# Kernel tuning notes

Measured on AMD Instinct MI355X. Metric: run time of the kernel, lower is better.

Reference implementation:

```python
import jax, jax.numpy as jnp
import numpy as np

DIMS = [128, 256, 512, 512]
RES = [64, 32, 16, 8]
B = 2
HEADS = 8
DH = 64
INNER = HEADS * DH  # 512


def setup_inputs() -> dict:
    key = jax.random.key(0)
    d = {}
    ctr = [0]
    def nk():
        ctr[0] += 1
        return jax.random.fold_in(key, ctr[0])
    for i, (c, r) in enumerate(zip(DIMS, RES)):
        for nm in ("ml_c", "ml_r", "fl_r"):
            d[f"{nm}{i}"] = jax.random.normal(nk(), (B, c, r, r), dtype=jnp.float32)
        for p in ("q", "k", "v"):
            d[f"w{p}{i}"] = jax.random.normal(nk(), (c, INNER), dtype=jnp.float32) * (c ** -0.5)
            d[f"b{p}{i}"] = jnp.zeros((INNER,), jnp.float32)
        d[f"wo{i}"] = jax.random.normal(nk(), (INNER, c), dtype=jnp.float32) * (INNER ** -0.5)
        d[f"bo{i}"] = jnp.zeros((c,), jnp.float32)
    return d


def _layer(xc, xr, xf, wq, bq, wk, bk, wv, bv, wo, bo):
    # xc/xr/xf: (B, C, H, W)
    Bb, C, H, W = xf.shape
    L = H * W
    flat = lambda t: t.reshape(Bb, C, L).transpose(0, 2, 1)          # (B, L, C)
    split = lambda t: t.reshape(Bb, L, HEADS, DH).transpose(0, 2, 1, 3)  # (B, h, L, d)
    q = split(flat(xc) @ wq + bq)
    k = split(flat(xr) @ wk + bk)
    v = split(flat(xf) @ wv + bv)
    attn = jax.nn.softmax(jnp.einsum('bhid,bhjd->bhij', q, k) * (DH ** -0.5), axis=-1)
    out = jnp.einsum('bhij,bhjd->bhid', attn, v)                      # (B, h, L, d)
    out = out.transpose(0, 2, 1, 3).reshape(Bb, L, INNER) @ wo + bo   # (B, L, C)
    return out.reshape(Bb, H, W, C).transpose(0, 3, 1, 2)             # (B, C, H, W)


def reference(ml_c0, ml_c1, ml_c2, ml_c3, ml_r0, ml_r1, ml_r2, ml_r3,
              fl_r0, fl_r1, fl_r2, fl_r3,
              wq0, bq0, wk0, bk0, wv0, bv0, wo0, bo0,
              wq1, bq1, wk1, bk1, wv1, bv1, wo1, bo1,
              wq2, bq2, wk2, bk2, wv2, bv2, wo2, bo2,
              wq3, bq3, wk3, bk3, wv3, bv3, wo3, bo3):
    mc = (ml_c0, ml_c1, ml_c2, ml_c3)
    mr = (ml_r0, ml_r1, ml_r2, ml_r3)
    fr = (fl_r0, fl_r1, fl_r2, fl_r3)
    ps = ((wq0, bq0, wk0, bk0, wv0, bv0, wo0, bo0),
          (wq1, bq1, wk1, bk1, wv1, bv1, wo1, bo1),
          (wq2, bq2, wk2, bk2, wv2, bv2, wo2, bo2),
          (wq3, bq3, wk3, bk3, wv3, bv3, wo3, bo3))
    return tuple(_layer(mc[i], mr[i], fr[i], *ps[i]) for i in range(4))
```

## Files before the change

kernel.cpp:

```cpp
#include <hip/hip_runtime.h>


typedef __attribute__((ext_vector_type(8))) short bf16x8;
typedef __attribute__((ext_vector_type(16))) float f32x16;
typedef __attribute__((ext_vector_type(4))) unsigned u32x4;
union BW { u32x4 u; bf16x8 b; };

#if __has_builtin(__builtin_amdgcn_exp2f)
#define EXP2F(x) __builtin_amdgcn_exp2f(x)
#else
#define EXP2F(x) exp2f(x)
#endif

__device__ __forceinline__ unsigned short f2bf(float f) {
    unsigned u = __float_as_uint(f);
    u += 0x7fffu + ((u >> 16) & 1u);
    return (unsigned short)(u >> 16);
}
__device__ __forceinline__ unsigned pack_bf16(float a, float b) {
    unsigned ua = __float_as_uint(a) + 0x8000u;
    unsigned ub = __float_as_uint(b) + 0x8000u;
#if __has_builtin(__builtin_amdgcn_perm)
    return __builtin_amdgcn_perm(ub, ua, 0x07060302u);
#else
    return (ua >> 16) | (ub & 0xffff0000u);
#endif
}

struct LayerP {
    unsigned short *xct, *xrt, *xft;
    unsigned short *wqt, *wkt, *wvt;
    unsigned short *wot;
    const float *bq, *bk, *bv, *bo;
    unsigned short *Qb, *Kb, *Vb, *Obt;
    float *out;
    int L, C;
};
struct Params {
    LayerP l[4];
    int xo128[5];
    int xoA[5];
};

struct Job { const float* src; unsigned short* dst; int R, C; };
struct PrepParams { Job jobs[40]; int off[41]; int njobs; };

__device__ __forceinline__ int layer_of(int bx, const int* xo) {
    return (bx >= xo[1]) + (bx >= xo[2]) + (bx >= xo[3]);
}

__global__ __launch_bounds__(256) void prep(PrepParams P)
{
    __shared__ float T[32][33];
    int bx = blockIdx.x, j = 0;
    while (j + 1 < P.njobs && bx >= P.off[j + 1]) ++j;
    const Job job = P.jobs[j];
    const int t = bx - P.off[j];
    const int rt = job.R >> 5;
    const int tr = t % rt, tc = t / rt;

    const int tid = threadIdx.x;
    const int c = tid & 31, rb = tid >> 5;
    const float* sp = job.src + (size_t)(tr * 32 + rb) * job.C + tc * 32 + c;
#pragma unroll
    for (int i = 0; i < 4; ++i)
        T[rb + 8 * i][c] = sp[(size_t)8 * i * job.C];
    __syncthreads();

    const int cp = tid & 15, dl = tid >> 4;
#pragma unroll
    for (int ph = 0; ph < 2; ++ph) {
        int d = dl + 16 * ph;
        unsigned v = pack_bf16(T[2 * cp][d], T[2 * cp + 1][d]);
        *(unsigned*)&job.dst[(size_t)(tc * 32 + d) * job.R + tr * 32 + 2 * cp] = v;
    }
}

__device__ __forceinline__ void gemm_bt_core(
        const unsigned short* __restrict__ At, int m0, int M,
        const unsigned short* __restrict__ Wt,
        int K, unsigned short* As, unsigned short* Ws, f32x16 (&acc)[2][2])
{
    const int tid = threadIdx.x;
    const int r = tid >> 1, half = tid & 1;
    const int rm = (m0 + r < M) ? (m0 + r) : (M - 1);
    const unsigned short* ap = At + (size_t)rm * K + half * 16;
    const unsigned short* wp = Wt + (size_t)r * K + half * 16;
    const int s = (r >> 3) & 3;
    const int wb0 = r * 40 + (((half * 2)     ^ s) << 3);
    const int wb1 = r * 40 + (((half * 2 + 1) ^ s) << 3);

    const int lane = tid & 63, wave = tid >> 6;
    const int q = lane & 31, h = lane >> 5;
    const int wm = (wave & 1) * 64, wn = (wave >> 1) * 64;

#pragma unroll
    for (int i = 0; i < 2; ++i)
#pragma unroll
        for (int jn = 0; jn < 2; ++jn)
#pragma unroll
            for (int e = 0; e < 16; ++e) acc[i][jn][e] = 0.f;

    uint4 a0 = *(const uint4*)ap,       a1 = *(const uint4*)(ap + 8);
    uint4 w0 = *(const uint4*)wp,       w1 = *(const uint4*)(wp + 8);

    for (int k0 = 0; k0 < K; k0 += 32) {
        __syncthreads();
        *(uint4*)&As[wb0] = a0;  *(uint4*)&As[wb1] = a1;
        *(uint4*)&Ws[wb0] = w0;  *(uint4*)&Ws[wb1] = w1;
        __syncthreads();
        if (k0 + 32 < K) {
            a0 = *(const uint4*)(ap + k0 + 32);  a1 = *(const uint4*)(ap + k0 + 40);
            w0 = *(const uint4*)(wp + k0 + 32);  w1 = *(const uint4*)(wp + k0 + 40);
        }
#pragma unroll
        for (int c = 0; c < 2; ++c) {
            bf16x8 af[2], bf[2];
#pragma unroll
            for (int im = 0; im < 2; ++im) {
                int rr = wm + im * 32 + q;
                af[im] = *(const bf16x8*)&As[rr * 40 + ((((c << 1) | h) ^ ((rr >> 3) & 3)) << 3)];
                int rn = wn + im * 32 + q;
                bf[im] = *(const bf16x8*)&Ws[rn * 40 + ((((c << 1) | h) ^ ((rn >> 3) & 3)) << 3)];
            }
#pragma unroll
            for (int im = 0; im < 2; ++im)
#pragma unroll
                for (int in = 0; in < 2; ++in)
                    acc[im][in] = __builtin_amdgcn_mfma_f32_32x32x16_bf16(
                        af[im], bf[in], acc[im][in], 0, 0, 0);
        }
    }
}

__global__ __launch_bounds__(256) void proj_qkv(Params P)
{
    __shared__ unsigned short As[128 * 40], Ws[128 * 40];
    const int bx = blockIdx.x;
    const int layer = layer_of(bx, P.xo128);
    const LayerP lp = P.l[layer];
    const int M = lp.L, K = lp.C;
    const int m0 = (bx - P.xo128[layer]) * 128;
    const int p = blockIdx.z >> 1, b = blockIdx.z & 1;
    const int n0 = blockIdx.y * 128;

    const unsigned short* At = (p == 0 ? lp.xct : p == 1 ? lp.xrt : lp.xft)
                               + (size_t)b * M * K;
    const unsigned short* Wt = (p == 0 ? lp.wqt : p == 1 ? lp.wkt : lp.wvt)
                               + (size_t)n0 * K;
    const float* bias = (p == 0 ? lp.bq : p == 1 ? lp.bk : lp.bv);

    f32x16 acc[2][2];
    gemm_bt_core(At, m0, M, Wt, K, As, Ws, acc);

    const int tid = threadIdx.x, lane = tid & 63, wave = tid >> 6;
    const int q = lane & 31, h = lane >> 5;
    const int wm = (wave & 1) * 64, wn = (wave >> 1) * 64;
    const int bh = b * 8 + (n0 >> 6) + (wn >> 6);

#pragma unroll
    for (int im = 0; im < 2; ++im) {
        const int m_base = m0 + wm + im * 32;
        if (m_base >= M) continue;
#pragma unroll
        for (int in = 0; in < 2; ++in) {
            const int d = in * 32 + q;
            const float bvv = bias[n0 + wn + d];
            const f32x16 A = acc[im][in];
            if (p <= 1) {
                const float sc = (p == 0) ? 0.18033688f : 1.f;
                const int ck = d >> 4, hk = (d >> 3) & 1, jk = d & 7;
                unsigned short* O = (p == 0 ? lp.Qb : lp.Kb)
                                  + (size_t)bh * (M / 32) * 2048
                                  + (size_t)((m_base >> 5) * 4 + ck) * 512 + hk * 8 + jk;
#pragma unroll
                for (int rg = 0; rg < 4; ++rg)
#pragma unroll
                    for (int i = 0; i < 4; ++i)
                        O[(rg * 8 + 4 * h + i) * 16] = f2bf((A[rg * 4 + i] + bvv) * sc);
            } else {
                unsigned short* O = lp.Vb + (size_t)bh * (M / 16) * 1024;
#pragma unroll
                for (int rg = 0; rg < 4; ++rg) {
                    int kc16 = (m_base >> 4) + (rg >> 1);
                    int j16 = (rg & 1) * 8 + 4 * h;
                    uint2 vv;
                    vv.x = pack_bf16(A[rg * 4 + 0] + bvv, A[rg * 4 + 1] + bvv);
                    vv.y = pack_bf16(A[rg * 4 + 2] + bvv, A[rg * 4 + 3] + bvv);
                    *(uint2*)(O + ((size_t)kc16 * 64 + d) * 16 + j16) = vv;
                }
            }
        }
    }
}

__global__ __launch_bounds__(256, 2) void attn(Params P)
{
    __shared__ float Os[2][32][68];
    __shared__ float Ls[4][2][64];
    __shared__ float Li[32];

    const int bx = blockIdx.x;
    const int layer = layer_of(bx, P.xoA);
    const LayerP lp = P.l[layer];
    const int L = lp.L;
    const int q0 = (bx - P.xoA[layer]) * 64;
    const int bh = blockIdx.y;

    const int tid = threadIdx.x, wave = tid >> 6, lane = tid & 63;
    const int q = lane & 31, h = lane >> 5;
    const bool hb = (h != 0);

    const unsigned short* Qbase = lp.Qb + (size_t)bh * (L / 32) * 2048 + q * 16 + h * 8;
    const unsigned short* Kbase = lp.Kb + (size_t)bh * (L / 32) * 2048 + q * 16 + h * 8;
    const unsigned short* Vbase = lp.Vb + (size_t)bh * (L / 16) * 1024 + q * 16 + h * 8;

    bf16x8 qf[2][4];
#pragma unroll
    for (int g = 0; g < 2; ++g)
#pragma unroll
        for (int c = 0; c < 4; ++c)
            qf[g][c] = *(const bf16x8*)(Qbase + (size_t)(q0 / 32 + g) * 2048 + c * 512);

    f32x16 o0[2], o1[2];
#pragma unroll
    for (int g = 0; g < 2; ++g)
#pragma unroll
        for (int i = 0; i < 16; ++i) { o0[g][i] = 0.f; o1[g][i] = 0.f; }
    float lacc[2] = {0.f, 0.f};

    const int nkt = L >> 6;
    for (int kt = wave; kt < nkt; kt += 4) {
        const unsigned short* kp0 = Kbase + (size_t)(kt * 2) * 2048;
        bf16x8 ka[4], kb_[4];
#pragma unroll
        for (int c = 0; c < 4; ++c) {
            ka[c]  = *(const bf16x8*)(kp0 + c * 512);
            kb_[c] = *(const bf16x8*)(kp0 + 2048 + c * 512);
        }
        const unsigned short* vp0 = Vbase + (size_t)(kt * 4) * 1024;
        bf16x8 va[4], vb[4];
#pragma unroll
        for (int kc = 0; kc < 4; ++kc) {
            va[kc] = *(const bf16x8*)(vp0 + kc * 1024);
            vb[kc] = *(const bf16x8*)(vp0 + kc * 1024 + 512);
        }

#pragma unroll
        for (int g = 0; g < 2; ++g) {
            f32x16 st0, st1;
#pragma unroll
            for (int i = 0; i < 16; ++i) { st0[i] = 0.f; st1[i] = 0.f; }
#pragma unroll
            for (int c = 0; c < 4; ++c) {
                st0 = __builtin_amdgcn_mfma_f32_32x32x16_bf16(ka[c],  qf[g][c], st0, 0, 0, 0);
                st1 = __builtin_amdgcn_mfma_f32_32x32x16_bf16(kb_[c], qf[g][c], st1, 0, 0, 0);
            }

            float ls = 0.f;
#pragma unroll
            for (int i = 0; i < 16; ++i) {
                st0[i] = EXP2F(st0[i]); ls += st0[i];
                st1[i] = EXP2F(st1[i]); ls += st1[i];
            }
            ls += __shfl_xor(ls, 32);
            lacc[g] += ls;

            unsigned pw0[8], pw1[8];
#pragma unroll
            for (int mt = 0; mt < 2; ++mt) {
                const f32x16 sM = mt ? st1 : st0;
#pragma unroll
                for (int rg = 0; rg < 4; ++rg) {
                    pw0[mt * 4 + rg] = pack_bf16(sM[rg * 4 + 0], sM[rg * 4 + 1]);
                    pw1[mt * 4 + rg] = pack_bf16(sM[rg * 4 + 2], sM[rg * 4 + 3]);
                }
            }

#pragma unroll
            for (int kc = 0; kc < 4; ++kc) {
                const int mt = kc >> 1, rb = (kc & 1) * 2;
                unsigned ownA = hb ? pw0[mt * 4 + rb + 1] : pw0[mt * 4 + rb];
                unsigned ownB = hb ? pw1[mt * 4 + rb + 1] : pw1[mt * 4 + rb];
                unsigned srcA = hb ? pw0[mt * 4 + rb]     : pw0[mt * 4 + rb + 1];
                unsigned srcB = hb ? pw1[mt * 4 + rb]     : pw1[mt * 4 + rb + 1];
                unsigned gotA = __shfl_xor(srcA, 32);
                unsigned gotB = __shfl_xor(srcB, 32);
                BW bw;
                bw.u[0] = hb ? gotA : ownA;
                bw.u[1] = hb ? gotB : ownB;
                bw.u[2] = hb ? ownA : gotA;
                bw.u[3] = hb ? ownB : gotB;
                o0[g] = __builtin_amdgcn_mfma_f32_32x32x16_bf16(va[kc], bw.b, o0[g], 0, 0, 0);
                o1[g] = __builtin_amdgcn_mfma_f32_32x32x16_bf16(vb[kc], bw.b, o1[g], 0, 0, 0);
            }
        }
    }

    Ls[wave][0][lane] = lacc[0];
    Ls[wave][1][lane] = lacc[1];

#pragma unroll 1
    for (int g = 0; g < 2; ++g) {
        __syncthreads();
        if (wave >= 2) {
#pragma unroll
            for (int r = 0; r < 16; ++r) {
                Os[wave - 2][r][lane]      = o0[g][r];
                Os[wave - 2][16 + r][lane] = o1[g][r];
            }
        }
        __syncthreads();
        if (wave < 2) {
#pragma unroll
            for (int r = 0; r < 16; ++r) {
                Os[wave][r][lane]      += o0[g][r];
                Os[wave][16 + r][lane] += o1[g][r];
            }
        }
        __syncthreads();
        if (tid < 32)
            Li[tid] = 1.f / (Ls[0][g][tid] + Ls[1][g][tid] + Ls[2][g][tid] + Ls[3][g][tid]);
        __syncthreads();

        const int d = tid >> 2, qg = (tid & 3) * 8;
        const int dm = d & 31;
        const int hh2 = (dm >> 2) & 1;
        const int R = ((dm & 3) | ((dm >> 3) << 2)) + ((d >= 32) ? 16 : 0);
        float v[8];
#pragma unroll
        for (int j = 0; j < 8; ++j)
            v[j] = (Os[0][R][hh2 * 32 + qg + j] + Os[1][R][hh2 * 32 + qg + j]) * Li[qg + j];
        __syncthreads();
#pragma unroll
        for (int j = 0; j < 8; ++j)
            ((float*)Os)[(qg + j) * 68 + d] = v[j];
        __syncthreads();
        {
            const int qq = tid >> 3, db = (tid & 7) * 8;
            const float* xp = &((float*)Os)[qq * 68 + db];
            u32x4 pk;
            pk[0] = pack_bf16(xp[0], xp[1]);
            pk[1] = pack_bf16(xp[2], xp[3]);
            pk[2] = pack_bf16(xp[4], xp[5]);
            pk[3] = pack_bf16(xp[6], xp[7]);
            const int bb = bh >> 3, hh = bh & 7;
            const int row = q0 + g * 32 + qq;
            *(u32x4*)(lp.Obt + ((size_t)bb * L + row) * 512 + hh * 64 + db) = pk;
        }
    }
}

__global__ __launch_bounds__(256) void proj_o(Params P)
{
    const int bx = blockIdx.x;
    const int layer = layer_of(bx, P.xo128);
    const LayerP lp = P.l[layer];
    const int M = lp.L, N = lp.C;
    const int n0 = blockIdx.y * 128;
    if (n0 >= N) return;
    __shared__ unsigned short As[128 * 40], Ws[128 * 40];
    const int m0 = (bx - P.xo128[layer]) * 128;
    const int b = blockIdx.z;

    f32x16 acc[2][2];
    gemm_bt_core(lp.Obt + (size_t)b * M * 512, m0, M,
                 lp.wot + (size_t)n0 * 512, 512, As, Ws, acc);

    const int tid = threadIdx.x, lane = tid & 63, wave = tid >> 6;
    const int q = lane & 31, h = lane >> 5;
    const int wm = (wave & 1) * 64, wn = (wave >> 1) * 64;

#pragma unroll
    for (int im = 0; im < 2; ++im) {
        const int m_base = m0 + wm + im * 32;
        if (m_base >= M) continue;
#pragma unroll
        for (int in = 0; in < 2; ++in) {
            const int n = n0 + wn + in * 32 + q;
            if (n >= N) continue;
            const float bvv = lp.bo[n];
            float* O = lp.out + ((size_t)b * N + n) * M;
            const f32x16 A = acc[im][in];
#pragma unroll
            for (int rg = 0; rg < 4; ++rg) {
                float vv[4];
#pragma unroll
                for (int i = 0; i < 4; ++i) vv[i] = A[rg * 4 + i] + bvv;
                *(float4*)(O + m_base + rg * 8 + 4 * h) = *(float4*)vv;
            }
        }
    }
}

static void build_prep(PrepParams& PP, const Params& P, int first, int last)
{
    int nj = 0, off = 0;
    for (int i = first; i < last; ++i) {
        const LayerP& lp = P.l[i];
        const int C = lp.C, L = lp.L;
        unsigned short* xd[3] = { lp.xct, lp.xrt, lp.xft };
        for (int tn = 0; tn < 3; ++tn)
            for (int b = 0; b < 2; ++b) {
                Job& J = PP.jobs[nj];
                J.dst = xd[tn] + (size_t)b * L * C;
                J.src = nullptr;
                J.R = C; J.C = L;
                PP.off[nj] = off; off += (C / 32) * (L / 32); ++nj;
            }
        unsigned short* wd[3] = { lp.wqt, lp.wkt, lp.wvt };
        for (int wn = 0; wn < 3; ++wn) {
            Job& J = PP.jobs[nj];
            J.dst = wd[wn]; J.src = nullptr; J.R = C; J.C = 512;
            PP.off[nj] = off; off += (C / 32) * 16; ++nj;
        }
        Job& J = PP.jobs[nj];
        J.dst = lp.wot; J.src = nullptr; J.R = 512; J.C = C;
        PP.off[nj] = off; off += 16 * (C / 32); ++nj;
    }
    PP.njobs = nj;
    PP.off[nj] = off;
}

extern "C" void kernel_launch(void* const* d_in, const int* in_sizes, int n_in,
                              void* d_out, int out_size, void* d_ws, size_t ws_size,
                              hipStream_t stream)
{
    static const int DIMS[4] = {128, 256, 512, 512};
    static const int RES[4]  = {64, 32, 16, 8};

    char* ws = (char*)d_ws;
    float* outf = (float*)d_out;

    Params P;
    const float* srcs[4][10];
    size_t out_off = 0;

    size_t qkv_tot = 0, xt_tot = 0, obt_tot = 0, w_tot = 0;
    int Ls_[4], Cs_[4];
    for (int i = 0; i < 4; ++i) {
        Ls_[i] = RES[i] * RES[i]; Cs_[i] = DIMS[i];
        qkv_tot += (size_t)6144 * Ls_[i];
        xt_tot  += (size_t)12 * Ls_[i] * Cs_[i];
        obt_tot += (size_t)2048 * Ls_[i];
        w_tot   += (size_t)4096 * Cs_[i];
    }
    size_t r2 = (xt_tot > obt_tot) ? xt_tot : obt_tot;
    const bool fits = qkv_tot + r2 + w_tot <= ws_size;

    auto fill_layer = [&](int i, size_t qkv_base, size_t xt_base, size_t obt_base,
                          size_t w_base) {
        const int C = Cs_[i], L = Ls_[i];
        LayerP& lp = P.l[i];
        for (int t = 0; t < 10; ++t) srcs[i][t] = nullptr;
        srcs[i][0] = (const float*)d_in[i * 11 + 0];
        srcs[i][1] = (const float*)d_in[i * 11 + 1];
        srcs[i][2] = (const float*)d_in[i * 11 + 2];
        srcs[i][3] = (const float*)d_in[i * 11 + 3];
        srcs[i][4] = (const float*)d_in[i * 11 + 5];
        srcs[i][5] = (const float*)d_in[i * 11 + 7];
        srcs[i][6] = (const float*)d_in[i * 11 + 9];
        lp.bq = (const float*)d_in[i * 11 + 4];
        lp.bk = (const float*)d_in[i * 11 + 6];
        lp.bv = (const float*)d_in[i * 11 + 8];
        lp.bo = (const float*)d_in[i * 11 + 10];
        lp.Qb  = (unsigned short*)(ws + qkv_base);
        lp.Kb  = (unsigned short*)(ws + qkv_base + (size_t)2048 * L);
        lp.Vb  = (unsigned short*)(ws + qkv_base + (size_t)4096 * L);
        lp.xct = (unsigned short*)(ws + xt_base);
        lp.xrt = (unsigned short*)(ws + xt_base + (size_t)4 * L * C);
        lp.xft = (unsigned short*)(ws + xt_base + (size_t)8 * L * C);
        lp.Obt = (unsigned short*)(ws + obt_base);
        lp.wqt = (unsigned short*)(ws + w_base);
        lp.wkt = (unsigned short*)(ws + w_base + (size_t)1024 * C);
        lp.wvt = (unsigned short*)(ws + w_base + (size_t)2048 * C);
        lp.wot = (unsigned short*)(ws + w_base + (size_t)3072 * C);
        lp.out = outf + out_off;
        lp.L = L; lp.C = C;
    };

    dim3 blk(256);

    if (fits) {
        size_t qb = 0, xb = qkv_tot, ob = qkv_tot, wb = qkv_tot + r2;
        P.xo128[0] = P.xoA[0] = 0;
        for (int i = 0; i < 4; ++i) {
            fill_layer(i, qb, xb, ob, wb);
            qb += (size_t)6144 * Ls_[i];
            xb += (size_t)12 * Ls_[i] * Cs_[i];
            ob += (size_t)2048 * Ls_[i];
            wb += (size_t)4096 * Cs_[i];
            out_off += (size_t)2 * Cs_[i] * Ls_[i];
            P.xo128[i + 1] = P.xo128[i] + (Ls_[i] + 127) / 128;
            P.xoA[i + 1]   = P.xoA[i] + Ls_[i] / 64;
        }
        PrepParams PP;
        build_prep(PP, P, 0, 4);
        {
            int nj = 0;
            for (int i = 0; i < 4; ++i) {
                for (int tn = 0; tn < 3; ++tn)
                    for (int b = 0; b < 2; ++b)
                        PP.jobs[nj++].src = srcs[i][tn] + (size_t)b * Cs_[i] * Ls_[i];
                for (int wn = 0; wn < 3; ++wn) PP.jobs[nj++].src = srcs[i][3 + wn];
                PP.jobs[nj++].src = srcs[i][6];
            }
        }
        prep    <<<dim3(PP.off[PP.njobs]), blk, 0, stream>>>(PP);
        proj_qkv<<<dim3(P.xo128[4], 4, 6), blk, 0, stream>>>(P);
        attn    <<<dim3(P.xoA[4], 16, 1), blk, 0, stream>>>(P);
        proj_o  <<<dim3(P.xo128[4], 4, 2), blk, 0, stream>>>(P);
    } else {
        for (int i = 0; i < 4; ++i) {
            const int L = Ls_[i], C = Cs_[i];
            size_t qb = 0;
            size_t xb = (size_t)6144 * L;
            size_t ob = xb;
            size_t r2i = (size_t)12 * L * C;
            if ((size_t)2048 * L > r2i) r2i = (size_t)2048 * L;
            size_t wb = xb + r2i;
            fill_layer(i, qb, xb, ob, wb);
            out_off += (size_t)2 * C * L;

            Params Pi;
            Pi.l[0] = P.l[i]; Pi.l[1] = P.l[i]; Pi.l[2] = P.l[i]; Pi.l[3] = P.l[i];
            Pi.xo128[0] = 0; Pi.xoA[0] = 0;
            for (int k = 1; k < 5; ++k) {
                Pi.xo128[k] = (L + 127) / 128;
                Pi.xoA[k]   = L / 64;
            }
            PrepParams PP;
            build_prep(PP, Pi, 0, 1);
            {
                int nj = 0;
                for (int tn = 0; tn < 3; ++tn)
                    for (int b = 0; b < 2; ++b)
                        PP.jobs[nj++].src = srcs[i][tn] + (size_t)b * C * L;
                for (int wn = 0; wn < 3; ++wn) PP.jobs[nj++].src = srcs[i][3 + wn];
                PP.jobs[nj++].src = srcs[i][6];
            }
            prep    <<<dim3(PP.off[PP.njobs]), blk, 0, stream>>>(PP);
            proj_qkv<<<dim3(Pi.xo128[4], 4, 6), blk, 0, stream>>>(Pi);
            attn    <<<dim3(Pi.xoA[4], 16, 1), blk, 0, stream>>>(Pi);
            proj_o  <<<dim3(Pi.xo128[4], 4, 2), blk, 0, stream>>>(Pi);
        }
    }
}
```

Baseline: 357.3 us.

## Shrink attention query tile to 32 rows per block and regroup workspace per layer

The attention kernel now handles 32 query rows per block instead of 64. This doubles the grid, drops the per-block loop over two query groups, and raises the occupancy hint from 2 to 3 blocks. The aim is more parallelism across CUs for the small layers and lower register pressure. In exchange, every K/V tile is loaded twice as often across blocks. The host code is also restructured to pack as many layers as fit into the workspace per launch group, overlaying Obt on the transposed-input region. Kernels are templated so each launch grouping gets its own instantiation.

```diff
diff --git a/kernel.cpp b/kernel.cpp
--- a/kernel.cpp
+++ b/kernel.cpp
@@ -39,7 +39,7 @@
 struct Params {
     LayerP l[4];
     int xo128[5];
-    int xoA[5];
+    int xo32[5];
 };
 
 struct Job { const float* src; unsigned short* dst; int R, C; };
@@ -49,6 +49,7 @@
     return (bx >= xo[1]) + (bx >= xo[2]) + (bx >= xo[3]);
 }
 
+template<int TAG>
 __global__ __launch_bounds__(256) void prep(PrepParams P)
 {
     __shared__ float T[32][33];
@@ -133,6 +134,7 @@
     }
 }
 
+template<int TAG>
 __global__ __launch_bounds__(256) void proj_qkv(Params P)
 {
     __shared__ unsigned short As[128 * 40], Ws[128 * 40];
@@ -194,17 +196,18 @@
     }
 }
 
-__global__ __launch_bounds__(256, 2) void attn(Params P)
+template<int TAG>
+__global__ __launch_bounds__(256, 3) void attn(Params P)
 {
     __shared__ float Os[2][32][68];
-    __shared__ float Ls[4][2][64];
+    __shared__ float Ls[4][64];
     __shared__ float Li[32];
 
     const int bx = blockIdx.x;
-    const int layer = layer_of(bx, P.xoA);
+    const int layer = layer_of(bx, P.xo32);
     const LayerP lp = P.l[layer];
     const int L = lp.L;
-    const int q0 = (bx - P.xoA[layer]) * 64;
+    const int q0 = (bx - P.xo32[layer]) * 32;
     const int bh = blockIdx.y;
 
     const int tid = threadIdx.x, wave = tid >> 6, lane = tid & 63;
@@ -215,19 +218,15 @@
     const unsigned short* Kbase = lp.Kb + (size_t)bh * (L / 32) * 2048 + q * 16 + h * 8;
     const unsigned short* Vbase = lp.Vb + (size_t)bh * (L / 16) * 1024 + q * 16 + h * 8;
 
-    bf16x8 qf[2][4];
-#pragma unroll
-    for (int g = 0; g < 2; ++g)
-#pragma unroll
-        for (int c = 0; c < 4; ++c)
-            qf[g][c] = *(const bf16x8*)(Qbase + (size_t)(q0 / 32 + g) * 2048 + c * 512);
-
-    f32x16 o0[2], o1[2];
-#pragma unroll
-    for (int g = 0; g < 2; ++g)
-#pragma unroll
-        for (int i = 0; i < 16; ++i) { o0[g][i] = 0.f; o1[g][i] = 0.f; }
-    float lacc[2] = {0.f, 0.f};
+    bf16x8 qf[4];
+#pragma unroll
+    for (int c = 0; c < 4; ++c)
+        qf[c] = *(const bf16x8*)(Qbase + (size_t)(q0 >> 5) * 2048 + c * 512);
+
+    f32x16 o0, o1;
+#pragma unroll
+    for (int i = 0; i < 16; ++i) { o0[i] = 0.f; o1[i] = 0.f; }
+    float lacc = 0.f;
 
     const int nkt = L >> 6;
     for (int kt = wave; kt < nkt; kt += 4) {
@@ -238,6 +237,15 @@
             ka[c]  = *(const bf16x8*)(kp0 + c * 512);
             kb_[c] = *(const bf16x8*)(kp0 + 2048 + c * 512);
         }
+        f32x16 st0, st1;
+#pragma unroll
+        for (int i = 0; i < 16; ++i) { st0[i] = 0.f; st1[i] = 0.f; }
+#pragma unroll
+        for (int c = 0; c < 4; ++c) {
+            st0 = __builtin_amdgcn_mfma_f32_32x32x16_bf16(ka[c],  qf[c], st0, 0, 0, 0);
+            st1 = __builtin_amdgcn_mfma_f32_32x32x16_bf16(kb_[c], qf[c], st1, 0, 0, 0);
+        }
+
         const unsigned short* vp0 = Vbase + (size_t)(kt * 4) * 1024;
         bf16x8 va[4], vb[4];
 #pragma unroll
@@ -246,111 +254,96 @@
             vb[kc] = *(const bf16x8*)(vp0 + kc * 1024 + 512);
         }
 
-#pragma unroll
-        for (int g = 0; g < 2; ++g) {
-            f32x16 st0, st1;
-#pragma unroll
-            for (int i = 0; i < 16; ++i) { st0[i] = 0.f; st1[i] = 0.f; }
-#pragma unroll
-            for (int c = 0; c < 4; ++c) {
-                st0 = __builtin_amdgcn_mfma_f32_32x32x16_bf16(ka[c],  qf[g][c], st0, 0, 0, 0);
-                st1 = __builtin_amdgcn_mfma_f32_32x32x16_bf16(kb_[c], qf[g][c], st1, 0, 0, 0);
+        float ls = 0.f;
+#pragma unroll
+        for (int i = 0; i < 16; ++i) {
+            st0[i] = EXP2F(st0[i]); ls += st0[i];
+            st1[i] = EXP2F(st1[i]); ls += st1[i];
+        }
+        lacc += ls;
+
+        unsigned pw0[8], pw1[8];
+#pragma unroll
+        for (int mt = 0; mt < 2; ++mt) {
+            const f32x16 sM = mt ? st1 : st0;
+#pragma unroll
+            for (int rg = 0; rg < 4; ++rg) {
+                pw0[mt * 4 + rg] = pack_bf16(sM[rg * 4 + 0], sM[rg * 4 + 1]);
+                pw1[mt * 4 + rg] = pack_bf16(sM[rg * 4 + 2], sM[rg * 4 + 3]);
             }
-
-            float ls = 0.f;
-#pragma unroll
-            for (int i = 0; i < 16; ++i) {
-                st0[i] = EXP2F(st0[i]); ls += st0[i];
-                st1[i] = EXP2F(st1[i]); ls += st1[i];
-            }
-            ls += __shfl_xor(ls, 32);
-            lacc[g] += ls;
-
-            unsigned pw0[8], pw1[8];
-#pragma unroll
-            for (int mt = 0; mt < 2; ++mt) {
-                const f32x16 sM = mt ? st1 : st0;
-#pragma unroll
-                for (int rg = 0; rg < 4; ++rg) {
-                    pw0[mt * 4 + rg] = pack_bf16(sM[rg * 4 + 0], sM[rg * 4 + 1]);
-                    pw1[mt * 4 + rg] = pack_bf16(sM[rg * 4 + 2], sM[rg * 4 + 3]);
-                }
-            }
-
-#pragma unroll
-            for (int kc = 0; kc < 4; ++kc) {
-                const int mt = kc >> 1, rb = (kc & 1) * 2;
-                unsigned ownA = hb ? pw0[mt * 4 + rb + 1] : pw0[mt * 4 + rb];
-                unsigned ownB = hb ? pw1[mt * 4 + rb + 1] : pw1[mt * 4 + rb];
-                unsigned srcA = hb ? pw0[mt * 4 + rb]     : pw0[mt * 4 + rb + 1];
-                unsigned srcB = hb ? pw1[mt * 4 + rb]     : pw1[mt * 4 + rb + 1];
-                unsigned gotA = __shfl_xor(srcA, 32);
-                unsigned gotB = __shfl_xor(srcB, 32);
-                BW bw;
-                bw.u[0] = hb ? gotA : ownA;
-                bw.u[1] = hb ? gotB : ownB;
-                bw.u[2] = hb ? ownA : gotA;
-                bw.u[3] = hb ? ownB : gotB;
-                o0[g] = __builtin_amdgcn_mfma_f32_32x32x16_bf16(va[kc], bw.b, o0[g], 0, 0, 0);
-                o1[g] = __builtin_amdgcn_mfma_f32_32x32x16_bf16(vb[kc], bw.b, o1[g], 0, 0, 0);
-            }
-        }
-    }
-
-    Ls[wave][0][lane] = lacc[0];
-    Ls[wave][1][lane] = lacc[1];
-
-#pragma unroll 1
-    for (int g = 0; g < 2; ++g) {
-        __syncthreads();
-        if (wave >= 2) {
-#pragma unroll
-            for (int r = 0; r < 16; ++r) {
-                Os[wave - 2][r][lane]      = o0[g][r];
-                Os[wave - 2][16 + r][lane] = o1[g][r];
-            }
-        }
-        __syncthreads();
-        if (wave < 2) {
-#pragma unroll
-            for (int r = 0; r < 16; ++r) {
-                Os[wave][r][lane]      += o0[g][r];
-                Os[wave][16 + r][lane] += o1[g][r];
-            }
-        }
-        __syncthreads();
-        if (tid < 32)
-            Li[tid] = 1.f / (Ls[0][g][tid] + Ls[1][g][tid] + Ls[2][g][tid] + Ls[3][g][tid]);
-        __syncthreads();
-
-        const int d = tid >> 2, qg = (tid & 3) * 8;
-        const int dm = d & 31;
-        const int hh2 = (dm >> 2) & 1;
-        const int R = ((dm & 3) | ((dm >> 3) << 2)) + ((d >= 32) ? 16 : 0);
-        float v[8];
-#pragma unroll
-        for (int j = 0; j < 8; ++j)
-            v[j] = (Os[0][R][hh2 * 32 + qg + j] + Os[1][R][hh2 * 32 + qg + j]) * Li[qg + j];
-        __syncthreads();
-#pragma unroll
-        for (int j = 0; j < 8; ++j)
-            ((float*)Os)[(qg + j) * 68 + d] = v[j];
-        __syncthreads();
-        {
-            const int qq = tid >> 3, db = (tid & 7) * 8;
-            const float* xp = &((float*)Os)[qq * 68 + db];
-            u32x4 pk;
-            pk[0] = pack_bf16(xp[0], xp[1]);
-            pk[1] = pack_bf16(xp[2], xp[3]);
-            pk[2] = pack_bf16(xp[4], xp[5]);
-            pk[3] = pack_bf16(xp[6], xp[7]);
-            const int bb = bh >> 3, hh = bh & 7;
-            const int row = q0 + g * 32 + qq;
-            *(u32x4*)(lp.Obt + ((size_t)bb * L + row) * 512 + hh * 64 + db) = pk;
-        }
-    }
-}
-
+        }
+
+#pragma unroll
+        for (int kc = 0; kc < 4; ++kc) {
+            const int mt = kc >> 1, rb = (kc & 1) * 2;
+            unsigned ownA = hb ? pw0[mt * 4 + rb + 1] : pw0[mt * 4 + rb];
+            unsigned ownB = hb ? pw1[mt * 4 + rb + 1] : pw1[mt * 4 + rb];
+            unsigned srcA = hb ? pw0[mt * 4 + rb]     : pw0[mt * 4 + rb + 1];
+            unsigned srcB = hb ? pw1[mt * 4 + rb]     : pw1[mt * 4 + rb + 1];
+            unsigned gotA = __shfl_xor(srcA, 32);
+            unsigned gotB = __shfl_xor(srcB, 32);
+            BW bw;
+            bw.u[0] = hb ? gotA : ownA;
+            bw.u[1] = hb ? gotB : ownB;
+            bw.u[2] = hb ? ownA : gotA;
+            bw.u[3] = hb ? ownB : gotB;
+            o0 = __builtin_amdgcn_mfma_f32_32x32x16_bf16(va[kc], bw.b, o0, 0, 0, 0);
+            o1 = __builtin_amdgcn_mfma_f32_32x32x16_bf16(vb[kc], bw.b, o1, 0, 0, 0);
+        }
+    }
+
+    Ls[wave][lane] = lacc;
+    if (wave >= 2) {
+#pragma unroll
+        for (int r = 0; r < 16; ++r) {
+            Os[wave - 2][r][lane]      = o0[r];
+            Os[wave - 2][16 + r][lane] = o1[r];
+        }
+    }
+    __syncthreads();
+    if (wave < 2) {
+#pragma unroll
+        for (int r = 0; r < 16; ++r) {
+            Os[wave][r][lane]      += o0[r];
+            Os[wave][16 + r][lane] += o1[r];
+        }
+    }
+    __syncthreads();
+    if (tid < 32) {
+        float s = 0.f;
+#pragma unroll
+        for (int w = 0; w < 4; ++w) s += Ls[w][tid] + Ls[w][32 + tid];
+        Li[tid] = 1.f / s;
+    }
+    __syncthreads();
+
+    const int d = tid >> 2, qg = (tid & 3) * 8;
+    const int dm = d & 31;
+    const int hh2 = (dm >> 2) & 1;
+    const int R = ((dm & 3) | ((dm >> 3) << 2)) + ((d >= 32) ? 16 : 0);
+    float v[8];
+#pragma unroll
+    for (int j = 0; j < 8; ++j)
+        v[j] = (Os[0][R][hh2 * 32 + qg + j] + Os[1][R][hh2 * 32 + qg + j]) * Li[qg + j];
+    __syncthreads();
+#pragma unroll
+    for (int j = 0; j < 8; ++j)
+        ((float*)Os)[(qg + j) * 68 + d] = v[j];
+    __syncthreads();
+    {
+        const int qq = tid >> 3, db = (tid & 7) * 8;
+        const float* xp = &((float*)Os)[qq * 68 + db];
+        u32x4 pk;
+        pk[0] = pack_bf16(xp[0], xp[1]);
+        pk[1] = pack_bf16(xp[2], xp[3]);
+        pk[2] = pack_bf16(xp[4], xp[5]);
+        pk[3] = pack_bf16(xp[6], xp[7]);
+        const int bb = bh >> 3, hh = bh & 7;
+        *(u32x4*)(lp.Obt + ((size_t)bb * L + q0 + qq) * 512 + hh * 64 + db) = pk;
+    }
+}
+
+template<int TAG>
 __global__ __launch_bounds__(256) void proj_o(Params P)
 {
     const int bx = blockIdx.x;
@@ -393,35 +386,6 @@
     }
 }
 
-static void build_prep(PrepParams& PP, const Params& P, int first, int last)
-{
-    int nj = 0, off = 0;
-    for (int i = first; i < last; ++i) {
-        const LayerP& lp = P.l[i];
-        const int C = lp.C, L = lp.L;
-        unsigned short* xd[3] = { lp.xct, lp.xrt, lp.xft };
-        for (int tn = 0; tn < 3; ++tn)
-            for (int b = 0; b < 2; ++b) {
-                Job& J = PP.jobs[nj];
-                J.dst = xd[tn] + (size_t)b * L * C;
-                J.src = nullptr;
-                J.R = C; J.C = L;
-                PP.off[nj] = off; off += (C / 32) * (L / 32); ++nj;
-            }
-        unsigned short* wd[3] = { lp.wqt, lp.wkt, lp.wvt };
-        for (int wn = 0; wn < 3; ++wn) {
-            Job& J = PP.jobs[nj];
-            J.dst = wd[wn]; J.src = nullptr; J.R = C; J.C = 512;
-            PP.off[nj] = off; off += (C / 32) * 16; ++nj;
-        }
-        Job& J = PP.jobs[nj];
-        J.dst = lp.wot; J.src = nullptr; J.R = 512; J.C = C;
-        PP.off[nj] = off; off += 16 * (C / 32); ++nj;
-    }
-    PP.njobs = nj;
-    PP.off[nj] = off;
-}
-
 extern "C" void kernel_launch(void* const* d_in, const int* in_sizes, int n_in,
                               void* d_out, int out_size, void* d_ws, size_t ws_size,
                               hipStream_t stream)
@@ -432,117 +396,122 @@
     char* ws = (char*)d_ws;
     float* outf = (float*)d_out;
 
-    Params P;
-    const float* srcs[4][10];
-    size_t out_off = 0;
-
-    size_t qkv_tot = 0, xt_tot = 0, obt_tot = 0, w_tot = 0;
     int Ls_[4], Cs_[4];
-    for (int i = 0; i < 4; ++i) {
-        Ls_[i] = RES[i] * RES[i]; Cs_[i] = DIMS[i];
-        qkv_tot += (size_t)6144 * Ls_[i];
-        xt_tot  += (size_t)12 * Ls_[i] * Cs_[i];
-        obt_tot += (size_t)2048 * Ls_[i];
-        w_tot   += (size_t)4096 * Cs_[i];
-    }
-    size_t r2 = (xt_tot > obt_tot) ? xt_tot : obt_tot;
-    const bool fits = qkv_tot + r2 + w_tot <= ws_size;
-
-    auto fill_layer = [&](int i, size_t qkv_base, size_t xt_base, size_t obt_base,
-                          size_t w_base) {
-        const int C = Cs_[i], L = Ls_[i];
-        LayerP& lp = P.l[i];
-        for (int t = 0; t < 10; ++t) srcs[i][t] = nullptr;
-        srcs[i][0] = (const float*)d_in[i * 11 + 0];
-        srcs[i][1] = (const float*)d_in[i * 11 + 1];
-        srcs[i][2] = (const float*)d_in[i * 11 + 2];
-        srcs[i][3] = (const float*)d_in[i * 11 + 3];
-        srcs[i][4] = (const float*)d_in[i * 11 + 5];
-        srcs[i][5] = (const float*)d_in[i * 11 + 7];
-        srcs[i][6] = (const float*)d_in[i * 11 + 9];
-        lp.bq = (const float*)d_in[i * 11 + 4];
-        lp.bk = (const float*)d_in[i * 11 + 6];
-        lp.bv = (const float*)d_in[i * 11 + 8];
-        lp.bo = (const float*)d_in[i * 11 + 10];
-        lp.Qb  = (unsigned short*)(ws + qkv_base);
-        lp.Kb  = (unsigned short*)(ws + qkv_base + (size_t)2048 * L);
-        lp.Vb  = (unsigned short*)(ws + qkv_base + (size_t)4096 * L);
-        lp.xct = (unsigned short*)(ws + xt_base);
-        lp.xrt = (unsigned short*)(ws + xt_base + (size_t)4 * L * C);
-        lp.xft = (unsigned short*)(ws + xt_base + (size_t)8 * L * C);
-        lp.Obt = (unsigned short*)(ws + obt_base);
-        lp.wqt = (unsigned short*)(ws + w_base);
-        lp.wkt = (unsigned short*)(ws + w_base + (size_t)1024 * C);
-        lp.wvt = (unsigned short*)(ws + w_base + (size_t)2048 * C);
-        lp.wot = (unsigned short*)(ws + w_base + (size_t)3072 * C);
-        lp.out = outf + out_off;
-        lp.L = L; lp.C = C;
+    const float* srcs[4][7];
+    const float* biases[4][4];
+    size_t out_offs[4];
+    {
+        size_t oo = 0;
+        for (int i = 0; i < 4; ++i) {
+            Ls_[i] = RES[i] * RES[i]; Cs_[i] = DIMS[i];
+            srcs[i][0] = (const float*)d_in[i * 11 + 0];
+            srcs[i][1] = (const float*)d_in[i * 11 + 1];
+            srcs[i][2] = (const float*)d_in[i * 11 + 2];
+            srcs[i][3] = (const float*)d_in[i * 11 + 3];
+            srcs[i][4] = (const float*)d_in[i * 11 + 5];
+            srcs[i][5] = (const float*)d_in[i * 11 + 7];
+            srcs[i][6] = (const float*)d_in[i * 11 + 9];
+            biases[i][0] = (const float*)d_in[i * 11 + 4];
+            biases[i][1] = (const float*)d_in[i * 11 + 6];
+            biases[i][2] = (const float*)d_in[i * 11 + 8];
+            biases[i][3] = (const float*)d_in[i * 11 + 10];
+            out_offs[i] = oo;
+            oo += (size_t)2 * Cs_[i] * Ls_[i];
+        }
+    }
+
+    auto foot = [&](int i) -> size_t {
+        size_t L = Ls_[i], C = Cs_[i];
+        size_t xt = 12 * L * C, ob = 2048 * L;
+        return 6144 * L + (xt > ob ? xt : ob) + 4096 * C;
     };
 
     dim3 blk(256);
 
-    if (fits) {
-        size_t qb = 0, xb = qkv_tot, ob = qkv_tot, wb = qkv_tot + r2;
-        P.xo128[0] = P.xoA[0] = 0;
-        for (int i = 0; i < 4; ++i) {
-            fill_layer(i, qb, xb, ob, wb);
-            qb += (size_t)6144 * Ls_[i];
-            xb += (size_t)12 * Ls_[i] * Cs_[i];
-            ob += (size_t)2048 * Ls_[i];
-            wb += (size_t)4096 * Cs_[i];
-            out_off += (size_t)2 * Cs_[i] * Ls_[i];
-            P.xo128[i + 1] = P.xo128[i] + (Ls_[i] + 127) / 128;
-            P.xoA[i + 1]   = P.xoA[i] + Ls_[i] / 64;
-        }
+    int start = 0;
+    while (start < 4) {
+        size_t tot = foot(start);
+        int end = start + 1;
+        while (end < 4 && tot + foot(end) <= ws_size) { tot += foot(end); ++end; }
+        const int n = end - start;
+
+        Params P;
+        P.xo128[0] = P.xo32[0] = 0;
+        size_t base = 0;
+        for (int j = 0; j < 4; ++j) {
+            if (j < n) {
+                const int i = start + j;
+                const size_t L = Ls_[i], C = Cs_[i];
+                LayerP& lp = P.l[j];
+                lp.Qb  = (unsigned short*)(ws + base);
+                lp.Kb  = (unsigned short*)(ws + base + 2048 * L);
+                lp.Vb  = (unsigned short*)(ws + base + 4096 * L);
+                const size_t xt0 = base + 6144 * L;
+                lp.xct = (unsigned short*)(ws + xt0);
+                lp.xrt = (unsigned short*)(ws + xt0 + 4 * L * C);
+                lp.xft = (unsigned short*)(ws + xt0 + 8 * L * C);
+                lp.Obt = (unsigned short*)(ws + xt0);
+                const size_t xtr = 12 * L * C, obr = 2048 * L;
+                const size_t w0 = xt0 + (xtr > obr ? xtr : obr);
+                lp.wqt = (unsigned short*)(ws + w0);
+                lp.wkt = (unsigned short*)(ws + w0 + 1024 * C);
+                lp.wvt = (unsigned short*)(ws + w0 + 2048 * C);
+                lp.wot = (unsigned short*)(ws + w0 + 3072 * C);
+                lp.bq = biases[i][0]; lp.bk = biases[i][1];
+                lp.bv = biases[i][2]; lp.bo = biases[i][3];
+                lp.out = outf + out_offs[i];
+                lp.L = (int)L; lp.C = (int)C;
+                base += foot(i);
+                P.xo128[j + 1] = P.xo128[j] + (Ls_[i] + 127) / 128;
+                P.xo32[j + 1]  = P.xo32[j] + Ls_[i] / 32;
+            } else {
+                P.l[j] = P.l[n - 1];
+                P.xo128[j + 1] = P.xo128[j];
+                P.xo32[j + 1]  = P.xo32[j];
+            }
+        }
+
         PrepParams PP;
-        build_prep(PP, P, 0, 4);
         {
-            int nj = 0;
-            for (int i = 0; i < 4; ++i) {
+            int nj = 0, off = 0;
+            for (int j = 0; j < n; ++j) {
+                const int i = start + j;
+                const int C = Cs_[i], L = Ls_[i];
+                const LayerP& lp = P.l[j];
+                unsigned short* xd[3] = { lp.xct, lp.xrt, lp.xft };
                 for (int tn = 0; tn < 3; ++tn)
-                    for (int b = 0; b < 2; ++b)
-                        PP.jobs[nj++].src = srcs[i][tn] + (size_t)b * Cs_[i] * Ls_[i];
-                for (int wn = 0; wn < 3; ++wn) PP.jobs[nj++].src = srcs[i][3 + wn];
-                PP.jobs[nj++].src = srcs[i][6];
+                    for (int b = 0; b < 2; ++b) {
+                        Job& J = PP.jobs[nj];
+                        J.dst = xd[tn] + (size_t)b * L * C;
+                        J.src = srcs[i][tn] + (size_t)b * C * L;
+                        J.R = C; J.C = L;
+                        PP.off[nj] = off; off += (C / 32) * (L / 32); ++nj;
+                    }
+                unsigned short* wd[3] = { lp.wqt, lp.wkt, lp.wvt };
+                for (int wn = 0; wn < 3; ++wn) {
+                    Job& J = PP.jobs[nj];
+                    J.dst = wd[wn]; J.src = srcs[i][3 + wn]; J.R = C; J.C = 512;
+                    PP.off[nj] = off; off += (C / 32) * 16; ++nj;
+                }
+                Job& J = PP.jobs[nj];
+                J.dst = lp.wot; J.src = srcs[i][6]; J.R = 512; J.C = C;
+                PP.off[nj] = off; off += 16 * (C / 32); ++nj;
             }
-        }
-        prep    <<<dim3(PP.off[PP.njobs]), blk, 0, stream>>>(PP);
-        proj_qkv<<<dim3(P.xo128[4], 4, 6), blk, 0, stream>>>(P);
-        attn    <<<dim3(P.xoA[4], 16, 1), blk, 0, stream>>>(P);
-        proj_o  <<<dim3(P.xo128[4], 4, 2), blk, 0, stream>>>(P);
-    } else {
-        for (int i = 0; i < 4; ++i) {
-            const int L = Ls_[i], C = Cs_[i];
-            size_t qb = 0;
-            size_t xb = (size_t)6144 * L;
-            size_t ob = xb;
-            size_t r2i = (size_t)12 * L * C;
-            if ((size_t)2048 * L > r2i) r2i = (size_t)2048 * L;
-            size_t wb = xb + r2i;
-            fill_layer(i, qb, xb, ob, wb);
-            out_off += (size_t)2 * C * L;
-
-            Params Pi;
-            Pi.l[0] = P.l[i]; Pi.l[1] = P.l[i]; Pi.l[2] = P.l[i]; Pi.l[3] = P.l[i];
-            Pi.xo128[0] = 0; Pi.xoA[0] = 0;
-            for (int k = 1; k < 5; ++k) {
-                Pi.xo128[k] = (L + 127) / 128;
-                Pi.xoA[k]   = L / 64;
-            }
-            PrepParams PP;
-            build_prep(PP, Pi, 0, 1);
-            {
-                int nj = 0;
-                for (int tn = 0; tn < 3; ++tn)
-                    for (int b = 0; b < 2; ++b)
-                        PP.jobs[nj++].src = srcs[i][tn] + (size_t)b * C * L;
-                for (int wn = 0; wn < 3; ++wn) PP.jobs[nj++].src = srcs[i][3 + wn];
-                PP.jobs[nj++].src = srcs[i][6];
-            }
-            prep    <<<dim3(PP.off[PP.njobs]), blk, 0, stream>>>(PP);
-            proj_qkv<<<dim3(Pi.xo128[4], 4, 6), blk, 0, stream>>>(Pi);
-            attn    <<<dim3(Pi.xoA[4], 16, 1), blk, 0, stream>>>(Pi);
-            proj_o  <<<dim3(Pi.xo128[4], 4, 2), blk, 0, stream>>>(Pi);
-        }
-    }
-}
+            PP.njobs = nj;
+            PP.off[nj] = off;
+        }
+
+        if (n == 4) {
+            prep<0>    <<<dim3(PP.off[PP.njobs]), blk, 0, stream>>>(PP);
+            proj_qkv<0><<<dim3(P.xo128[4], 4, 6), blk, 0, stream>>>(P);
+            attn<0>    <<<dim3(P.xo32[4], 16, 1), blk, 0, stream>>>(P);
+            proj_o<0>  <<<dim3(P.xo128[4], 4, 2), blk, 0, stream>>>(P);
+        } else {
+            prep<1>    <<<dim3(PP.off[PP.njobs]), blk, 0, stream>>>(PP);
+            proj_qkv<1><<<dim3(P.xo128[4], 4, 6), blk, 0, stream>>>(P);
+            attn<1>    <<<dim3(P.xo32[4], 16, 1), blk, 0, stream>>>(P);
+            proj_o<1>  <<<dim3(P.xo128[4], 4, 2), blk, 0, stream>>>(P);
+        }
+        start = end;
+    }
+}
```

Result: slower. 385.4 us (+7.9%).
